# Kernel optimization log

Hardware: AMD Instinct MI355X
Metric: run time of the kernel (lower is better)

The kernel has to match this reference:

```python
import jax, jax.numpy as jnp
import numpy as np
import math

S, E, D, H = 2048, 1024, 64, 16  # seq, embedding_dim (=D*H), per-head d_model, heads


def setup_inputs() -> dict:
    ks = jax.random.split(jax.random.key(0), 14)
    u = lambda k, sh: jax.random.uniform(k, sh, dtype=jnp.float32)
    n = lambda k, sh, s=0.02: s * jax.random.normal(k, sh, dtype=jnp.float32)
    return {
        "x": jax.random.normal(ks[0], (S, E), dtype=jnp.float32),
        # nn.Parameter(torch.rand(d_model, embedding_dim))
        "Wk": u(ks[1], (D, E)),
        "Wq": u(ks[2], (D, E)),
        "Wv": u(ks[3], (D, E)),
        # per-head Linear(d_model, d_model): weight [out,in]=[D,D], bias [D]
        "hWk": n(ks[4], (H, D, D)), "hbk": n(ks[5], (H, D)),
        "hWv": n(ks[6], (H, D, D)), "hbv": n(ks[7], (H, D)),
        "hWq": n(ks[8], (H, D, D)), "hbq": n(ks[9], (H, D)),
        # last_linear: Linear(D*H, D*H)
        "Wo": n(ks[10], (E, E)), "bo": n(ks[11], (E,)),
        # LayerNorm(D*H)
        "gamma": jnp.ones((E,), jnp.float32),
        "beta": jnp.zeros((E,), jnp.float32),
    }


def reference(x, Wk, Wq, Wv, hWk, hbk, hWv, hbv, hWq, hbq, Wo, bo, gamma, beta):
    # shared projections: [S, E] @ [E, D] -> [S, D]
    K = x @ Wk.T
    Q = x @ Wq.T
    V = x @ Wv.T
    # per-head linears (torch Linear: y = x @ W.T + b), vectorized over heads
    Kh = jnp.einsum('sd,hed->hse', K, hWk) + hbk[:, None, :]  # [H, S, D]
    Vh = jnp.einsum('sd,hed->hse', V, hWv) + hbv[:, None, :]
    Qh = jnp.einsum('sd,hed->hse', Q, hWq) + hbq[:, None, :]
    # scaled dot product attention; scale uses sqrt(d_model)
    scores = jnp.einsum('hqd,hkd->hqk', Qh, Kh) / math.sqrt(D)  # [H, S, S]
    attn = jax.nn.softmax(scores, axis=-1)
    O = jnp.einsum('hqk,hkd->hqd', attn, Vh)  # [H, S, D]
    # concat heads along feature dim (head order) -> [S, H*D]
    cat = jnp.transpose(O, (1, 0, 2)).reshape(S, H * D)
    out = cat @ Wo.T + bo
    # residual + LayerNorm (eps 1e-5)
    y = out + x
    mu = jnp.mean(y, axis=-1, keepdims=True)
    var = jnp.mean(jnp.square(y - mu), axis=-1, keepdims=True)
    return (y - mu) * jax.lax.rsqrt(var + 1e-5) * gamma + beta
```

## Files before the change

### kernel.cpp

```cpp
#include <hip/hip_runtime.h>
#include <math.h>

#define S 2048
#define E 1024
#define D 64
#define H 16

using f16 = _Float16;
typedef _Float16 v8h __attribute__((ext_vector_type(8)));
typedef _Float16 v4h __attribute__((ext_vector_type(4)));
typedef float v4f __attribute__((ext_vector_type(4)));

#define QSCALE (0.125f * 1.44269504f)

__device__ __forceinline__ float fexp2(float x) { return __builtin_amdgcn_exp2f(x); }

__device__ __forceinline__ void glds16(const f16* g, f16* l) {
    __builtin_amdgcn_global_load_lds(
        (const __attribute__((address_space(1))) void*)g,
        (__attribute__((address_space(3))) void*)l, 16, 0, 0);
}

__global__ void prep(const float* __restrict__ x, const float* __restrict__ Wo,
                     const float* __restrict__ hWk, const float* __restrict__ hWq,
                     const float* __restrict__ hWv,
                     const float* __restrict__ Wk, const float* __restrict__ Wq,
                     const float* __restrict__ Wv,
                     f16* __restrict__ Xh, f16* __restrict__ WoB,
                     f16* __restrict__ Wc) {
    __shared__ f16 Ah[64][72];
    __shared__ f16 Bt[64][72];
    const int t = threadIdx.x;

    if (blockIdx.x < 3072) {
        const size_t i = (size_t)blockIdx.x * 256 + t;
        const size_t NX = (size_t)S * E / 4;
        if (i < NX) {
            v4f w = ((const v4f*)x)[i];
            v4h h = {(f16)w[0], (f16)w[1], (f16)w[2], (f16)w[3]};
            ((v4h*)Xh)[i] = h;
        } else {
            const size_t j = i - NX;
            v4f w = ((const v4f*)Wo)[j];
            v4h h = {(f16)w[0], (f16)w[1], (f16)w[2], (f16)w[3]};
            ((v4h*)WoB)[j] = h;
        }
        return;
    }

    const int bb = blockIdx.x - 3072;
    const int th = bb >> 4;
    const int type = th >> 4, h = th & 15;
    const int e0 = (bb & 15) * 64;
    const float* hW = ((type == 0) ? hWk : (type == 1) ? hWq : hWv) + (size_t)h * D * D;
    const float* W  = (type == 0) ? Wk : (type == 1) ? Wq : Wv;

    {
        const int r16 = t >> 4, c4 = (t & 15) * 4;
#pragma unroll
        for (int rep = 0; rep < 4; ++rep) {
            const int row = rep * 16 + r16;
            v4f a = *(const v4f*)&hW[(size_t)row * D + c4];
#pragma unroll
            for (int j = 0; j < 4; ++j) Ah[row][c4 + j] = (f16)a[j];
            v4f w = *(const v4f*)&W[(size_t)row * E + e0 + c4];
#pragma unroll
            for (int j = 0; j < 4; ++j) Bt[c4 + j][row] = (f16)w[j];
        }
    }
    __syncthreads();

    const int wave = t >> 6, lane = t & 63;
    const int quad = lane >> 4, l16 = lane & 15;
    v4f acc[4] = {};
#pragma unroll
    for (int ks = 0; ks < 2; ++ks) {
        v8h af = *(const v8h*)&Ah[wave * 16 + l16][ks * 32 + quad * 8];
#pragma unroll
        for (int nt = 0; nt < 4; ++nt) {
            v8h bf = *(const v8h*)&Bt[nt * 16 + l16][ks * 32 + quad * 8];
            acc[nt] = __builtin_amdgcn_mfma_f32_16x16x32_f16(af, bf, acc[nt], 0, 0, 0);
        }
    }
#pragma unroll
    for (int r = 0; r < 4; ++r) {
        const int e2 = wave * 16 + quad * 4 + r;
#pragma unroll
        for (int nt = 0; nt < 4; ++nt)
            Wc[((size_t)th * D + e2) * E + e0 + nt * 16 + l16] = (f16)acc[nt][r];
    }
}

__global__ __launch_bounds__(256) void qkv_gemm(
        const f16* __restrict__ Xh, const f16* __restrict__ Wc,
        const float* __restrict__ hbk, const float* __restrict__ hbq,
        const float* __restrict__ hbv,
        f16* __restrict__ Kh, f16* __restrict__ Qh, f16* __restrict__ VhT) {
    const int m0 = blockIdx.x * 128;
    const int n0 = blockIdx.y * 64;
    const int type = n0 >> 10, h = (n0 >> 6) & 15;
    const float* hb = ((type == 0) ? hbk : (type == 1) ? hbq : hbv) + h * D;

    const int t = threadIdx.x;
    const int wave = t >> 6, lane = t & 63;
    const int quad = lane >> 4, l16 = lane & 15;
    const int wm = wave >> 1, wn = wave & 1;

    __shared__ f16 As[128 * 64];
    __shared__ f16 Bs[64 * 64];

    v4f acc[4][2] = {};
    const int lrow8 = lane >> 3, lg = lane & 7;

    for (int k0 = 0; k0 < E; k0 += 64) {
        __syncthreads();
#pragma unroll
        for (int jj = 0; jj < 4; ++jj) {
            const int j = wave * 4 + jj;
            const int row = j * 8 + lrow8;
            const int g = lg ^ (row & 7);
            glds16(Xh + (size_t)(m0 + row) * E + k0 + g * 8, &As[j * 512]);
        }
#pragma unroll
        for (int jj = 0; jj < 2; ++jj) {
            const int j = wave * 2 + jj;
            const int row = j * 8 + lrow8;
            const int g = lg ^ (row & 7);
            glds16(Wc + (size_t)(n0 + row) * E + k0 + g * 8, &Bs[j * 512]);
        }
        __syncthreads();

#pragma unroll
        for (int ks = 0; ks < 2; ++ks) {
            v8h a[4], b[2];
#pragma unroll
            for (int mt = 0; mt < 4; ++mt) {
                const int row = wm * 64 + mt * 16 + l16;
                a[mt] = *(const v8h*)&As[row * 64 + (((ks * 4 + quad) ^ (row & 7)) * 8)];
            }
#pragma unroll
            for (int nt = 0; nt < 2; ++nt) {
                const int row = wn * 32 + nt * 16 + l16;
                b[nt] = *(const v8h*)&Bs[row * 64 + (((ks * 4 + quad) ^ (row & 7)) * 8)];
            }
#pragma unroll
            for (int mt = 0; mt < 4; ++mt)
#pragma unroll
                for (int nt = 0; nt < 2; ++nt)
                    acc[mt][nt] = __builtin_amdgcn_mfma_f32_16x16x32_f16(a[mt], b[nt], acc[mt][nt], 0, 0, 0);
        }
    }

    if (type == 2) {
#pragma unroll
        for (int mt = 0; mt < 4; ++mt)
#pragma unroll
            for (int nt = 0; nt < 2; ++nt) {
                const int d = wn * 32 + nt * 16 + l16;
                const int s = m0 + wm * 64 + mt * 16 + quad * 4;
                const float b = hb[d];
                v4h vh;
#pragma unroll
                for (int r = 0; r < 4; ++r) vh[r] = (f16)(acc[mt][nt][r] + b);
                *(v4h*)(VhT + ((size_t)h * D + d) * S + s) = vh;
            }
    } else {
        f16* outp = (type == 0) ? Kh : Qh;
        const float osc = (type == 1) ? QSCALE : 1.f;
#pragma unroll
        for (int mt = 0; mt < 4; ++mt)
#pragma unroll
            for (int r = 0; r < 4; ++r) {
                const int s = m0 + wm * 64 + mt * 16 + quad * 4 + r;
#pragma unroll
                for (int nt = 0; nt < 2; ++nt) {
                    const int d = wn * 32 + nt * 16 + l16;
                    outp[((size_t)h * S + s) * D + d] = (f16)((acc[mt][nt][r] + hb[d]) * osc);
                }
            }
    }
}

#define NSPLIT 4
#define KSPAN (S / NSPLIT)
#define ITERS (KSPAN / 64)
#define PPAD 72

__global__ __launch_bounds__(256, 5) void attn_mfma(
        const f16* __restrict__ Qh, const f16* __restrict__ Kh,
        const f16* __restrict__ VhT, f16* __restrict__ Opart,
        float* __restrict__ ml) {
    const int h = blockIdx.y;
    const int q0 = blockIdx.x * 64;
    const int sp = blockIdx.z;
    const int t = threadIdx.x;
    const int wave = t >> 6, lane = t & 63;
    const int quad = lane >> 4, l16 = lane & 15;

    __shared__ f16 Kt[64 * 64];
    __shared__ f16 Vt[80 * 64];
    __shared__ union { f16 P[4][16][PPAD]; f16 O[64][PPAD]; } PO;

    {
        v4h one = {(f16)1, (f16)1, (f16)1, (f16)1};
        *(v4h*)&Vt[64 * 64 + t * 4] = one;
    }

    const int qrow = q0 + wave * 16 + l16;
    v8h qf[2];
    {
        const v8h* qp = (const v8h*)(Qh + ((size_t)h * S + qrow) * D);
        qf[0] = qp[quad];
        qf[1] = qp[quad + 4];
    }

    v4f oc[5] = {};
    float m_run = -INFINITY;
    const int kb = sp * KSPAN;
    const int srow = lane >> 3, sg = lane & 7;

    for (int it = 0; it < ITERS; ++it) {
        __syncthreads();
#pragma unroll
        for (int half = 0; half < 2; ++half) {
            const int row = wave * 16 + half * 8 + srow;
            const int g = sg ^ (row & 7);
            glds16(Kh + ((size_t)h * S + kb + it * 64 + row) * D + g * 8,
                   &Kt[(wave * 16 + half * 8) * 64]);
            glds16(VhT + ((size_t)h * D + row) * S + kb + it * 64 + g * 8,
                   &Vt[(wave * 16 + half * 8) * 64]);
        }
        __syncthreads();

        v4f sc[4] = {};
#pragma unroll
        for (int ks = 0; ks < 2; ++ks)
#pragma unroll
            for (int mt = 0; mt < 4; ++mt) {
                const int key = mt * 16 + l16;
                v8h kf = *(const v8h*)&Kt[key * 64 + (((ks * 4 + quad) ^ (key & 7)) * 8)];
                sc[mt] = __builtin_amdgcn_mfma_f32_16x16x32_f16(kf, qf[ks], sc[mt], 0, 0, 0);
            }

        float a0 = fmaxf(sc[0][0], sc[0][1]), a1 = fmaxf(sc[0][2], sc[0][3]);
        float a2 = fmaxf(sc[1][0], sc[1][1]), a3 = fmaxf(sc[1][2], sc[1][3]);
        float a4 = fmaxf(sc[2][0], sc[2][1]), a5 = fmaxf(sc[2][2], sc[2][3]);
        float a6 = fmaxf(sc[3][0], sc[3][1]), a7 = fmaxf(sc[3][2], sc[3][3]);
        float b0 = fmaxf(a0, a1), b1 = fmaxf(a2, a3);
        float b2 = fmaxf(a4, a5), b3 = fmaxf(a6, a7);
        float v = fmaxf(fmaxf(b0, b1), fmaxf(b2, b3));
        v = fmaxf(v, __shfl_xor(v, 16));
        v = fmaxf(v, __shfl_xor(v, 32));
        const float mnew = fmaxf(m_run, v);
        const float alpha = fexp2(m_run - mnew);
        m_run = mnew;
#pragma unroll
        for (int i = 0; i < 5; ++i) oc[i] *= alpha;

#pragma unroll
        for (int mt = 0; mt < 4; ++mt) {
            const float p0 = fexp2(sc[mt][0] - mnew);
            const float p1 = fexp2(sc[mt][1] - mnew);
            const float p2 = fexp2(sc[mt][2] - mnew);
            const float p3 = fexp2(sc[mt][3] - mnew);
            auto lo = __builtin_amdgcn_cvt_pkrtz(p0, p1);
            auto hi = __builtin_amdgcn_cvt_pkrtz(p2, p3);
            v4h ph; ph[0] = lo[0]; ph[1] = lo[1]; ph[2] = hi[0]; ph[3] = hi[1];
            *(v4h*)&PO.P[wave][l16][mt * 16 + quad * 4] = ph;
        }

#pragma unroll
        for (int ks = 0; ks < 2; ++ks) {
            v8h pf = *(const v8h*)&PO.P[wave][l16][ks * 32 + quad * 8];
#pragma unroll
            for (int mt = 0; mt < 5; ++mt) {
                const int dr = mt * 16 + l16;
                v8h vf = *(const v8h*)&Vt[dr * 64 + (((ks * 4 + quad) ^ (dr & 7)) * 8)];
                oc[mt] = __builtin_amdgcn_mfma_f32_16x16x32_f16(vf, pf, oc[mt], 0, 0, 0);
            }
        }
    }

    const float l = oc[4][0];
    const float invl = 1.f / l;
    __syncthreads();
#pragma unroll
    for (int mt = 0; mt < 4; ++mt) {
        auto lo = __builtin_amdgcn_cvt_pkrtz(oc[mt][0] * invl, oc[mt][1] * invl);
        auto hi = __builtin_amdgcn_cvt_pkrtz(oc[mt][2] * invl, oc[mt][3] * invl);
        v4h oh; oh[0] = lo[0]; oh[1] = lo[1]; oh[2] = hi[0]; oh[3] = hi[1];
        *(v4h*)&PO.O[wave * 16 + l16][mt * 16 + quad * 4] = oh;
    }
    if (quad == 0) {
        float* mlp = ml + (((size_t)sp * H + h) * S + qrow) * 2;
        mlp[0] = m_run;
        mlp[1] = l;
    }
    __syncthreads();
    {
        const int q = t >> 2, dg = (t & 3) * 16;
        v8h o0 = *(const v8h*)&PO.O[q][dg];
        v8h o1 = *(const v8h*)&PO.O[q][dg + 8];
        f16* dst = Opart + (((size_t)sp * H + h) * S + q0 + q) * D + dg;
        *(v8h*)dst = o0;
        *(v8h*)(dst + 8) = o1;
    }
}

__global__ void attn_combine(const f16* __restrict__ Opart,
                             const float* __restrict__ ml,
                             f16* __restrict__ cat) {
    const int q = blockIdx.x;
    const int t = threadIdx.x;
    const int idx = t * 4;
    const int h = idx >> 6, d0 = idx & 63;

    float m[NSPLIT], lv[NSPLIT];
    float M = -INFINITY;
#pragma unroll
    for (int sp = 0; sp < NSPLIT; ++sp) {
        const float* mlp = ml + (((size_t)sp * H + h) * S + q) * 2;
        m[sp] = mlp[0]; lv[sp] = mlp[1];
        M = fmaxf(M, m[sp]);
    }
    float asum = 0.f;
    float o[4] = {0.f, 0.f, 0.f, 0.f};
#pragma unroll
    for (int sp = 0; sp < NSPLIT; ++sp) {
        const float a = fexp2(m[sp] - M) * lv[sp];
        asum += a;
        v4h op = *(const v4h*)(Opart + (((size_t)sp * H + h) * S + q) * D + d0);
#pragma unroll
        for (int j = 0; j < 4; ++j) o[j] += a * (float)op[j];
    }
    const float inv = 1.f / asum;
    v4h co;
#pragma unroll
    for (int j = 0; j < 4; ++j) co[j] = (f16)(o[j] * inv);
    *(v4h*)(cat + (size_t)q * E + idx) = co;
}

__global__ __launch_bounds__(256) void gemm_y(
        const f16* __restrict__ cat, const f16* __restrict__ WoB,
        const float* __restrict__ bo, const f16* __restrict__ Xh,
        f16* __restrict__ y) {
    const int m0 = blockIdx.x * 64;
    const int n0 = blockIdx.y * 64;
    const int t = threadIdx.x;
    const int wave = t >> 6, lane = t & 63;
    const int quad = lane >> 4, l16 = lane & 15;
    const int wm = wave >> 1, wn = wave & 1;

    __shared__ f16 As[64 * 64];
    __shared__ f16 Bs[64 * 64];

    v4f acc[2][2] = {};
    const int lrow8 = lane >> 3, lg = lane & 7;

    for (int k0 = 0; k0 < E; k0 += 64) {
        __syncthreads();
#pragma unroll
        for (int jj = 0; jj < 2; ++jj) {
            const int j = wave * 2 + jj;
            const int row = j * 8 + lrow8;
            const int g = lg ^ (row & 7);
            glds16(cat + (size_t)(m0 + row) * E + k0 + g * 8, &As[j * 512]);
            glds16(WoB + (size_t)(n0 + row) * E + k0 + g * 8, &Bs[j * 512]);
        }
        __syncthreads();

#pragma unroll
        for (int ks = 0; ks < 2; ++ks) {
            v8h a[2], b[2];
#pragma unroll
            for (int mt = 0; mt < 2; ++mt) {
                const int row = wm * 32 + mt * 16 + l16;
                a[mt] = *(const v8h*)&As[row * 64 + (((ks * 4 + quad) ^ (row & 7)) * 8)];
            }
#pragma unroll
            for (int nt = 0; nt < 2; ++nt) {
                const int row = wn * 32 + nt * 16 + l16;
                b[nt] = *(const v8h*)&Bs[row * 64 + (((ks * 4 + quad) ^ (row & 7)) * 8)];
            }
#pragma unroll
            for (int mt = 0; mt < 2; ++mt)
#pragma unroll
                for (int nt = 0; nt < 2; ++nt)
                    acc[mt][nt] = __builtin_amdgcn_mfma_f32_16x16x32_f16(a[mt], b[nt], acc[mt][nt], 0, 0, 0);
        }
    }

#pragma unroll
    for (int mt = 0; mt < 2; ++mt)
#pragma unroll
        for (int r = 0; r < 4; ++r) {
            const int m = m0 + wm * 32 + mt * 16 + quad * 4 + r;
#pragma unroll
            for (int nt = 0; nt < 2; ++nt) {
                const int e = n0 + wn * 32 + nt * 16 + l16;
                y[(size_t)m * E + e] =
                    (f16)(acc[mt][nt][r] + bo[e] + (float)Xh[(size_t)m * E + e]);
            }
        }
}

__global__ void ln(const f16* __restrict__ y,
                   const float* __restrict__ gamma,
                   const float* __restrict__ beta,
                   float* __restrict__ out) {
    const int s = blockIdx.x;
    const int t = threadIdx.x;
    __shared__ float red[256];

    v4h yh = *(const v4h*)(y + (size_t)s * E + t * 4);
    float yv[4];
#pragma unroll
    for (int i = 0; i < 4; ++i) yv[i] = (float)yh[i];

    red[t] = yv[0] + yv[1] + yv[2] + yv[3];
    __syncthreads();
    for (int w = 128; w > 0; w >>= 1) {
        if (t < w) red[t] += red[t + w];
        __syncthreads();
    }
    const float mu = red[0] * (1.f / E);
    __syncthreads();

    float lv = 0.f;
#pragma unroll
    for (int i = 0; i < 4; ++i) { float dd = yv[i] - mu; lv += dd * dd; }
    red[t] = lv;
    __syncthreads();
    for (int w = 128; w > 0; w >>= 1) {
        if (t < w) red[t] += red[t + w];
        __syncthreads();
    }
    const float rstd = rsqrtf(red[0] * (1.f / E) + 1e-5f);

    v4f o;
#pragma unroll
    for (int i = 0; i < 4; ++i) {
        const int e = t * 4 + i;
        o[i] = (yv[i] - mu) * rstd * gamma[e] + beta[e];
    }
    *(v4f*)(out + (size_t)s * E + t * 4) = o;
}

extern "C" void kernel_launch(void* const* d_in, const int* in_sizes, int n_in,
                              void* d_out, int out_size, void* d_ws, size_t ws_size,
                              hipStream_t stream) {
    const float* x     = (const float*)d_in[0];
    const float* Wk    = (const float*)d_in[1];
    const float* Wq    = (const float*)d_in[2];
    const float* Wv    = (const float*)d_in[3];
    const float* hWk   = (const float*)d_in[4];
    const float* hbk   = (const float*)d_in[5];
    const float* hWv   = (const float*)d_in[6];
    const float* hbv   = (const float*)d_in[7];
    const float* hWq   = (const float*)d_in[8];
    const float* hbq   = (const float*)d_in[9];
    const float* Wo    = (const float*)d_in[10];
    const float* bo    = (const float*)d_in[11];
    const float* gamma = (const float*)d_in[12];
    const float* beta  = (const float*)d_in[13];
    float* out = (float*)d_out;

    char* base = (char*)d_ws;
    const size_t MB = 1u << 20;
    f16*   Kh    = (f16*)(base);
    f16*   Qh    = (f16*)(base + 4 * MB);
    f16*   VhT   = (f16*)(base + 8 * MB);
    f16*   Opart = (f16*)(base + 12 * MB);
    float* ml    = (float*)(base + 28 * MB);
    f16*   WoB   = (f16*)(base + 29 * MB);
    f16*   Xh    = (f16*)(base + 31 * MB);
    f16*   Wc    = (f16*)(base + 35 * MB);
    f16*   cat   = (f16*)(base + 41 * MB);
    f16*   y     = (f16*)(base + 45 * MB);

    prep<<<3072 + 768, 256, 0, stream>>>(x, Wo, hWk, hWq, hWv, Wk, Wq, Wv,
                                         Xh, WoB, Wc);
    qkv_gemm<<<dim3(S / 128, 3 * H * D / 64), 256, 0, stream>>>(Xh, Wc, hbk, hbq, hbv,
                                                                Kh, Qh, VhT);
    attn_mfma<<<dim3(S / 64, H, NSPLIT), 256, 0, stream>>>(Qh, Kh, VhT, Opart, ml);
    attn_combine<<<S, 256, 0, stream>>>(Opart, ml, cat);
    gemm_y<<<dim3(S / 64, E / 64), 256, 0, stream>>>(cat, WoB, bo, Xh, y);
    ln<<<S, 256, 0, stream>>>(y, gamma, beta, out);
}
```

Measured before the change: 170.1 us.

## Process two 16-query groups per wave in attention to reuse K/V tiles

The attention block now covers 128 queries instead of 64: each wave handles two 16-row query groups and reuses every K and V fragment it reads from shared memory for two MFMAs. This halves the number of K/V tiles loaded from global memory and shared memory per query, and halves the grid size. It costs twice the accumulator registers, so occupancy drops (launch bounds lowered from 5 to 4), and the grid shrinks to 16x16x4 = 1024 blocks, which may leave the GPU less evenly filled.

```diff
diff --git a/kernel.cpp b/kernel.cpp
--- a/kernel.cpp
+++ b/kernel.cpp
@@ -186,12 +186,12 @@
 #define ITERS (KSPAN / 64)
 #define PPAD 72
 
-__global__ __launch_bounds__(256, 5) void attn_mfma(
+__global__ __launch_bounds__(256, 4) void attn_mfma(
         const f16* __restrict__ Qh, const f16* __restrict__ Kh,
         const f16* __restrict__ VhT, f16* __restrict__ Opart,
         float* __restrict__ ml) {
     const int h = blockIdx.y;
-    const int q0 = blockIdx.x * 64;
+    const int q0 = blockIdx.x * 128;
     const int sp = blockIdx.z;
     const int t = threadIdx.x;
     const int wave = t >> 6, lane = t & 63;
@@ -199,23 +199,24 @@
 
     __shared__ f16 Kt[64 * 64];
     __shared__ f16 Vt[80 * 64];
-    __shared__ union { f16 P[4][16][PPAD]; f16 O[64][PPAD]; } PO;
+    __shared__ union { f16 P[4][32][PPAD]; f16 O[128][PPAD]; } PO;
 
     {
         v4h one = {(f16)1, (f16)1, (f16)1, (f16)1};
         *(v4h*)&Vt[64 * 64 + t * 4] = one;
     }
 
-    const int qrow = q0 + wave * 16 + l16;
-    v8h qf[2];
-    {
-        const v8h* qp = (const v8h*)(Qh + ((size_t)h * S + qrow) * D);
-        qf[0] = qp[quad];
-        qf[1] = qp[quad + 4];
-    }
-
-    v4f oc[5] = {};
-    float m_run = -INFINITY;
+    const int qbase = q0 + wave * 32;
+    v8h qf[2][2];
+#pragma unroll
+    for (int g = 0; g < 2; ++g) {
+        const v8h* qp = (const v8h*)(Qh + ((size_t)h * S + qbase + g * 16 + l16) * D);
+        qf[g][0] = qp[quad];
+        qf[g][1] = qp[quad + 4];
+    }
+
+    v4f oc[2][5] = {};
+    float m_run[2] = {-INFINITY, -INFINITY};
     const int kb = sp * KSPAN;
     const int srow = lane >> 3, sg = lane & 7;
 
@@ -232,78 +233,93 @@
         }
         __syncthreads();
 
-        v4f sc[4] = {};
+        v4f sc[2][4] = {};
 #pragma unroll
         for (int ks = 0; ks < 2; ++ks)
 #pragma unroll
             for (int mt = 0; mt < 4; ++mt) {
                 const int key = mt * 16 + l16;
                 v8h kf = *(const v8h*)&Kt[key * 64 + (((ks * 4 + quad) ^ (key & 7)) * 8)];
-                sc[mt] = __builtin_amdgcn_mfma_f32_16x16x32_f16(kf, qf[ks], sc[mt], 0, 0, 0);
-            }
-
-        float a0 = fmaxf(sc[0][0], sc[0][1]), a1 = fmaxf(sc[0][2], sc[0][3]);
-        float a2 = fmaxf(sc[1][0], sc[1][1]), a3 = fmaxf(sc[1][2], sc[1][3]);
-        float a4 = fmaxf(sc[2][0], sc[2][1]), a5 = fmaxf(sc[2][2], sc[2][3]);
-        float a6 = fmaxf(sc[3][0], sc[3][1]), a7 = fmaxf(sc[3][2], sc[3][3]);
-        float b0 = fmaxf(a0, a1), b1 = fmaxf(a2, a3);
-        float b2 = fmaxf(a4, a5), b3 = fmaxf(a6, a7);
-        float v = fmaxf(fmaxf(b0, b1), fmaxf(b2, b3));
-        v = fmaxf(v, __shfl_xor(v, 16));
-        v = fmaxf(v, __shfl_xor(v, 32));
-        const float mnew = fmaxf(m_run, v);
-        const float alpha = fexp2(m_run - mnew);
-        m_run = mnew;
-#pragma unroll
-        for (int i = 0; i < 5; ++i) oc[i] *= alpha;
-
-#pragma unroll
-        for (int mt = 0; mt < 4; ++mt) {
-            const float p0 = fexp2(sc[mt][0] - mnew);
-            const float p1 = fexp2(sc[mt][1] - mnew);
-            const float p2 = fexp2(sc[mt][2] - mnew);
-            const float p3 = fexp2(sc[mt][3] - mnew);
-            auto lo = __builtin_amdgcn_cvt_pkrtz(p0, p1);
-            auto hi = __builtin_amdgcn_cvt_pkrtz(p2, p3);
-            v4h ph; ph[0] = lo[0]; ph[1] = lo[1]; ph[2] = hi[0]; ph[3] = hi[1];
-            *(v4h*)&PO.P[wave][l16][mt * 16 + quad * 4] = ph;
+#pragma unroll
+                for (int g = 0; g < 2; ++g)
+                    sc[g][mt] = __builtin_amdgcn_mfma_f32_16x16x32_f16(kf, qf[g][ks], sc[g][mt], 0, 0, 0);
+            }
+
+#pragma unroll
+        for (int g = 0; g < 2; ++g) {
+            float a0 = fmaxf(sc[g][0][0], sc[g][0][1]), a1 = fmaxf(sc[g][0][2], sc[g][0][3]);
+            float a2 = fmaxf(sc[g][1][0], sc[g][1][1]), a3 = fmaxf(sc[g][1][2], sc[g][1][3]);
+            float a4 = fmaxf(sc[g][2][0], sc[g][2][1]), a5 = fmaxf(sc[g][2][2], sc[g][2][3]);
+            float a6 = fmaxf(sc[g][3][0], sc[g][3][1]), a7 = fmaxf(sc[g][3][2], sc[g][3][3]);
+            float b0 = fmaxf(a0, a1), b1 = fmaxf(a2, a3);
+            float b2 = fmaxf(a4, a5), b3 = fmaxf(a6, a7);
+            float v = fmaxf(fmaxf(b0, b1), fmaxf(b2, b3));
+            v = fmaxf(v, __shfl_xor(v, 16));
+            v = fmaxf(v, __shfl_xor(v, 32));
+            const float mnew = fmaxf(m_run[g], v);
+            const float alpha = fexp2(m_run[g] - mnew);
+            m_run[g] = mnew;
+#pragma unroll
+            for (int i = 0; i < 5; ++i) oc[g][i] *= alpha;
+#pragma unroll
+            for (int mt = 0; mt < 4; ++mt) {
+                const float p0 = fexp2(sc[g][mt][0] - mnew);
+                const float p1 = fexp2(sc[g][mt][1] - mnew);
+                const float p2 = fexp2(sc[g][mt][2] - mnew);
+                const float p3 = fexp2(sc[g][mt][3] - mnew);
+                auto lo = __builtin_amdgcn_cvt_pkrtz(p0, p1);
+                auto hi = __builtin_amdgcn_cvt_pkrtz(p2, p3);
+                v4h ph; ph[0] = lo[0]; ph[1] = lo[1]; ph[2] = hi[0]; ph[3] = hi[1];
+                *(v4h*)&PO.P[wave][g * 16 + l16][mt * 16 + quad * 4] = ph;
+            }
         }
 
 #pragma unroll
         for (int ks = 0; ks < 2; ++ks) {
-            v8h pf = *(const v8h*)&PO.P[wave][l16][ks * 32 + quad * 8];
+            v8h pf[2];
+#pragma unroll
+            for (int g = 0; g < 2; ++g)
+                pf[g] = *(const v8h*)&PO.P[wave][g * 16 + l16][ks * 32 + quad * 8];
 #pragma unroll
             for (int mt = 0; mt < 5; ++mt) {
                 const int dr = mt * 16 + l16;
                 v8h vf = *(const v8h*)&Vt[dr * 64 + (((ks * 4 + quad) ^ (dr & 7)) * 8)];
-                oc[mt] = __builtin_amdgcn_mfma_f32_16x16x32_f16(vf, pf, oc[mt], 0, 0, 0);
-            }
-        }
-    }
-
-    const float l = oc[4][0];
-    const float invl = 1.f / l;
+#pragma unroll
+                for (int g = 0; g < 2; ++g)
+                    oc[g][mt] = __builtin_amdgcn_mfma_f32_16x16x32_f16(vf, pf[g], oc[g][mt], 0, 0, 0);
+            }
+        }
+    }
+
     __syncthreads();
 #pragma unroll
-    for (int mt = 0; mt < 4; ++mt) {
-        auto lo = __builtin_amdgcn_cvt_pkrtz(oc[mt][0] * invl, oc[mt][1] * invl);
-        auto hi = __builtin_amdgcn_cvt_pkrtz(oc[mt][2] * invl, oc[mt][3] * invl);
-        v4h oh; oh[0] = lo[0]; oh[1] = lo[1]; oh[2] = hi[0]; oh[3] = hi[1];
-        *(v4h*)&PO.O[wave * 16 + l16][mt * 16 + quad * 4] = oh;
-    }
-    if (quad == 0) {
-        float* mlp = ml + (((size_t)sp * H + h) * S + qrow) * 2;
-        mlp[0] = m_run;
-        mlp[1] = l;
+    for (int g = 0; g < 2; ++g) {
+        const float l = oc[g][4][0];
+        const float invl = 1.f / l;
+#pragma unroll
+        for (int mt = 0; mt < 4; ++mt) {
+            auto lo = __builtin_amdgcn_cvt_pkrtz(oc[g][mt][0] * invl, oc[g][mt][1] * invl);
+            auto hi = __builtin_amdgcn_cvt_pkrtz(oc[g][mt][2] * invl, oc[g][mt][3] * invl);
+            v4h oh; oh[0] = lo[0]; oh[1] = lo[1]; oh[2] = hi[0]; oh[3] = hi[1];
+            *(v4h*)&PO.O[wave * 32 + g * 16 + l16][mt * 16 + quad * 4] = oh;
+        }
+        if (quad == 0) {
+            float* mlp = ml + (((size_t)sp * H + h) * S + qbase + g * 16 + l16) * 2;
+            mlp[0] = m_run[g];
+            mlp[1] = l;
+        }
     }
     __syncthreads();
     {
-        const int q = t >> 2, dg = (t & 3) * 16;
-        v8h o0 = *(const v8h*)&PO.O[q][dg];
-        v8h o1 = *(const v8h*)&PO.O[q][dg + 8];
+        const int q = t >> 1, dg = (t & 1) * 32;
         f16* dst = Opart + (((size_t)sp * H + h) * S + q0 + q) * D + dg;
-        *(v8h*)dst = o0;
-        *(v8h*)(dst + 8) = o1;
+#pragma unroll
+        for (int c = 0; c < 4; c += 2) {
+            v8h o0 = *(const v8h*)&PO.O[q][dg + c * 8];
+            v8h o1 = *(const v8h*)&PO.O[q][dg + c * 8 + 8];
+            *(v8h*)(dst + c * 8) = o0;
+            *(v8h*)(dst + c * 8 + 8) = o1;
+        }
     }
 }
 
@@ -482,7 +498,7 @@
                                          Xh, WoB, Wc);
     qkv_gemm<<<dim3(S / 128, 3 * H * D / 64), 256, 0, stream>>>(Xh, Wc, hbk, hbq, hbv,
                                                                 Kh, Qh, VhT);
-    attn_mfma<<<dim3(S / 64, H, NSPLIT), 256, 0, stream>>>(Qh, Kh, VhT, Opart, ml);
+    attn_mfma<<<dim3(S / 128, H, NSPLIT), 256, 0, stream>>>(Qh, Kh, VhT, Opart, ml);
     attn_combine<<<S, 256, 0, stream>>>(Opart, ml, cat);
     gemm_y<<<dim3(S / 64, E / 64), 256, 0, stream>>>(cat, WoB, bo, Xh, y);
     ln<<<S, 256, 0, stream>>>(y, gamma, beta, out);
```

New measurement: 169.7 us. No clear change (-0.3%).
